# Performance work log

Hardware: AMD Instinct MI355X
Metric: run time of the kernel (lower is better)

The kernel has to match this reference:

```python
import jax, jax.numpy as jnp
import numpy as np

EPS = 1e-8  # torch CosineSimilarity default eps
IN_DIM = 4096
OUT_DIM = 32768
BATCH = 4096


def setup_inputs() -> dict:
    key = jax.random.key(0)
    kx, kw = jax.random.split(key)
    x = jax.random.normal(kx, (BATCH, IN_DIM), dtype=jnp.float32)
    # kaiming_normal_ on a (1, in, out) tensor: fan_in = in * out (last-dim fan), std = sqrt(2/fan_in)
    std = np.sqrt(2.0 / (IN_DIM * OUT_DIM)).astype(np.float32)
    weight = jax.random.normal(kw, (IN_DIM, OUT_DIM), dtype=jnp.float32) * std
    return {"x": x, "weight": weight}


def reference(x, weight):
    # cosine similarity along the in_dim axis between each row of x and each
    # column of weight: dot(x, w) / (max(||x||, eps) * max(||w||, eps))
    dots = jnp.einsum("bi,io->bo", x, weight)              # (B, out)
    x_norm = jnp.maximum(jnp.linalg.norm(x, axis=1), EPS)  # (B,)
    w_norm = jnp.maximum(jnp.linalg.norm(weight, axis=0), EPS)  # (out,)
    return dots / (x_norm[:, None] * w_norm[None, :])
```

## Files before the change

### kernel.cpp

```cpp
#include <hip/hip_runtime.h>
#include <hip/hip_bf16.h>
#include <cstdint>
#include <cstddef>

#define IN_DIM 4096
#define OUT_DIM 32768
#define BATCH 4096
#define EPS 1e-8f

typedef __attribute__((ext_vector_type(4))) float f32x4;
typedef __attribute__((ext_vector_type(8))) short bf16x8;

__device__ __forceinline__ unsigned short f2bf(float f) {
    union { float f; unsigned int u; } v;
    v.f = f;
    unsigned int u = v.u;
    unsigned int r = (u + 0x7FFFu + ((u >> 16) & 1u)) >> 16;
    return (unsigned short)r;
}

__device__ __forceinline__ void load_lds16(const void* g, void* l) {
    __builtin_amdgcn_global_load_lds(
        (const __attribute__((address_space(1))) void*)g,
        (__attribute__((address_space(3))) void*)l,
        16, 0, 0);
}

__global__ void xprep(const float* __restrict__ x,
                      unsigned short* __restrict__ xb,
                      float* __restrict__ xinv) {
    const int row = blockIdx.x;
    const int tid = threadIdx.x;
    const float4* x4 = (const float4*)(x + (size_t)row * IN_DIM);
    ushort4* xb4 = (ushort4*)(xb + (size_t)row * IN_DIM);
    float ss = 0.f;
#pragma unroll
    for (int it = 0; it < IN_DIM / 4 / 256; ++it) {
        int i = it * 256 + tid;
        float4 v = x4[i];
        ss += v.x * v.x + v.y * v.y + v.z * v.z + v.w * v.w;
        ushort4 o;
        o.x = f2bf(v.x); o.y = f2bf(v.y); o.z = f2bf(v.z); o.w = f2bf(v.w);
        xb4[i] = o;
    }
#pragma unroll
    for (int off = 32; off > 0; off >>= 1) ss += __shfl_down(ss, off);
    __shared__ float red[4];
    if ((tid & 63) == 0) red[tid >> 6] = ss;
    __syncthreads();
    if (tid == 0) {
        float s = red[0] + red[1] + red[2] + red[3];
        xinv[row] = 1.f / fmaxf(sqrtf(s), EPS);
    }
}

__global__ void wprep(const float* __restrict__ w,
                      unsigned short* __restrict__ wt,
                      float* __restrict__ wn2) {
    __shared__ unsigned short tile[64][66];
    __shared__ float colsum[64];
    const int t = threadIdx.x;
    const int j0 = blockIdx.x * 64;
    const int i0 = blockIdx.y * 64;
    if (t < 64) colsum[t] = 0.f;
    __syncthreads();

    const int jj = t & 63;
    const int ibase = t >> 6;
    float ss = 0.f;
#pragma unroll
    for (int it = 0; it < 16; ++it) {
        int ii = it * 4 + ibase;
        float v = w[(size_t)(i0 + ii) * OUT_DIM + j0 + jj];
        ss += v * v;
        tile[ii][jj] = f2bf(v);
    }
    atomicAdd(&colsum[jj], ss);
    __syncthreads();
    if (t < 64) atomicAdd(&wn2[j0 + t], colsum[t]);

    const int ii2 = t & 63;
    const int jbase = t >> 6;
#pragma unroll
    for (int it = 0; it < 16; ++it) {
        int jj2 = it * 4 + jbase;
        wt[(size_t)(j0 + jj2) * IN_DIM + i0 + ii2] = tile[ii2][jj2];
    }
}

__global__ void wfin(const float* __restrict__ wn2, float* __restrict__ winv) {
    int j = blockIdx.x * 256 + threadIdx.x;
    winv[j] = 1.f / fmaxf(sqrtf(wn2[j]), EPS);
}

#define BM 128
#define BN 128
#define BK 32

__global__ void gemm_kernel(const unsigned short* __restrict__ A,
                            const unsigned short* __restrict__ B,
                            float* __restrict__ C,
                            const float* __restrict__ xinv,
                            const float* __restrict__ winv) {
    __shared__ unsigned short As[BM * BK];
    __shared__ unsigned short Bs[BN * BK];

    const int tid = threadIdx.x;
    const int wave = tid >> 6;
    const int lane = tid & 63;
    const int m0 = blockIdx.x * BM;
    const int n0 = blockIdx.y * BN;
    const int wm = (wave & 1) * 64;
    const int wn = (wave >> 1) * 64;

    f32x4 acc[4][4] = {};

    const int lrow = lane >> 2;
    const int lk = (lane & 3) * 8;

    const int ml = lane & 15;
    const int quad = lane >> 4;

    for (int k0 = 0; k0 < IN_DIM; k0 += BK) {
#pragma unroll
        for (int l = 0; l < 2; ++l) {
            int grow = l * 64 + wave * 16 + lrow;
            const unsigned short* gpa = A + (size_t)(m0 + grow) * IN_DIM + k0 + lk;
            unsigned short* lpa = As + (size_t)(l * 256 + wave * 64) * 8;
            load_lds16(gpa, lpa);
            const unsigned short* gpb = B + (size_t)(n0 + grow) * IN_DIM + k0 + lk;
            unsigned short* lpb = Bs + (size_t)(l * 256 + wave * 64) * 8;
            load_lds16(gpb, lpb);
        }
        __syncthreads();

        bf16x8 af[4], bfr[4];
#pragma unroll
        for (int i = 0; i < 4; ++i) {
            af[i] = *(const bf16x8*)&As[(wm + i * 16 + ml) * BK + quad * 8];
            bfr[i] = *(const bf16x8*)&Bs[(wn + i * 16 + ml) * BK + quad * 8];
        }
#pragma unroll
        for (int i = 0; i < 4; ++i)
#pragma unroll
            for (int j = 0; j < 4; ++j)
                acc[i][j] = __builtin_amdgcn_mfma_f32_16x16x32_bf16(
                    af[i], bfr[j], acc[i][j], 0, 0, 0);
        __syncthreads();
    }

    float xs[4][4];
#pragma unroll
    for (int i = 0; i < 4; ++i)
#pragma unroll
        for (int r = 0; r < 4; ++r)
            xs[i][r] = xinv[m0 + wm + i * 16 + quad * 4 + r];

#pragma unroll
    for (int j = 0; j < 4; ++j) {
        int n = n0 + wn + j * 16 + ml;
        float wsc = winv[n];
#pragma unroll
        for (int i = 0; i < 4; ++i) {
            int mbase = m0 + wm + i * 16 + quad * 4;
#pragma unroll
            for (int r = 0; r < 4; ++r) {
                C[(size_t)(mbase + r) * OUT_DIM + n] = acc[i][j][r] * wsc * xs[i][r];
            }
        }
    }
}

extern "C" void kernel_launch(void* const* d_in, const int* in_sizes, int n_in,
                              void* d_out, int out_size, void* d_ws, size_t ws_size,
                              hipStream_t stream) {
    const float* x = (const float*)d_in[0];
    const float* w = (const float*)d_in[1];
    float* out = (float*)d_out;

    char* ws = (char*)d_ws;
    unsigned short* xb = (unsigned short*)ws;
    unsigned short* wt = (unsigned short*)(ws + (size_t)BATCH * IN_DIM * 2);
    char* tail = ws + (size_t)BATCH * IN_DIM * 2 + (size_t)OUT_DIM * IN_DIM * 2;
    float* xinv = (float*)tail;
    float* wn2 = xinv + BATCH;
    float* winv = wn2 + OUT_DIM;

    hipMemsetAsync(wn2, 0, OUT_DIM * sizeof(float), stream);
    xprep<<<BATCH, 256, 0, stream>>>(x, xb, xinv);
    wprep<<<dim3(OUT_DIM / 64, IN_DIM / 64), 256, 0, stream>>>(w, wt, wn2);
    wfin<<<OUT_DIM / 256, 256, 0, stream>>>(wn2, winv);
    gemm_kernel<<<dim3(BATCH / BM, OUT_DIM / BN), 256, 0, stream>>>(xb, wt, out, xinv, winv);
}
```

Baseline: 2.100 ms.

## Rewrite GEMM with 256x256 tiles, 4-stage LDS pipeline, swizzle; vectorize wprep

The GEMM moves to 256x256 block tiles with 8 waves, a 4-deep ring of LDS buffers filled by asynchronous global-to-LDS loads, and an XOR swizzle on LDS addresses to avoid bank conflicts. It also remaps block IDs for better L2 locality and raises wave priority around the MFMA sections. The weight prep kernel now uses float4 loads, packed 16-byte transposed stores and fewer atomics per column. The costs are 128KB of dynamic LDS per block, higher register pressure from the doubled accumulators, and complex hand-written wait counts that must be exactly right to stay correct.

```diff
diff --git a/kernel.cpp b/kernel.cpp
--- a/kernel.cpp
+++ b/kernel.cpp
@@ -10,6 +10,7 @@
 
 typedef __attribute__((ext_vector_type(4))) float f32x4;
 typedef __attribute__((ext_vector_type(8))) short bf16x8;
+typedef __attribute__((ext_vector_type(4))) unsigned int u32x4;
 
 __device__ __forceinline__ unsigned short f2bf(float f) {
     union { float f; unsigned int u; } v;
@@ -57,34 +58,59 @@
 __global__ void wprep(const float* __restrict__ w,
                       unsigned short* __restrict__ wt,
                       float* __restrict__ wn2) {
-    __shared__ unsigned short tile[64][66];
-    __shared__ float colsum[64];
+    __shared__ unsigned int tile32[64][33];
+    __shared__ f32x4 csum[256];
     const int t = threadIdx.x;
     const int j0 = blockIdx.x * 64;
-    const int i0 = blockIdx.y * 64;
-    if (t < 64) colsum[t] = 0.f;
+    const int kb = blockIdx.y * 512;
+    const int c4 = t & 15;
+    const int ir = t >> 4;
+    f32x4 ss = {0.f, 0.f, 0.f, 0.f};
+#pragma unroll 1
+    for (int tk = 0; tk < 8; ++tk) {
+        const int i0 = kb + tk * 64;
+#pragma unroll
+        for (int p = 0; p < 4; ++p) {
+            int il = p * 16 + ir;
+            const float4 v = *(const float4*)(w + (size_t)(i0 + il) * OUT_DIM + j0 + c4 * 4);
+            ss[0] += v.x * v.x; ss[1] += v.y * v.y;
+            ss[2] += v.z * v.z; ss[3] += v.w * v.w;
+            tile32[il][c4 * 2]     = (unsigned int)f2bf(v.x) | ((unsigned int)f2bf(v.y) << 16);
+            tile32[il][c4 * 2 + 1] = (unsigned int)f2bf(v.z) | ((unsigned int)f2bf(v.w) << 16);
+        }
+        __syncthreads();
+#pragma unroll
+        for (int e = 0; e < 2; ++e) {
+            int idx = e * 256 + t;
+            int jj = idx >> 3;
+            int ch = idx & 7;
+            unsigned int sh = (jj & 1) * 16;
+            int cc = jj >> 1;
+            unsigned int u0 = (tile32[ch * 8 + 0][cc] >> sh) & 0xffffu;
+            unsigned int u1 = (tile32[ch * 8 + 1][cc] >> sh) & 0xffffu;
+            unsigned int u2 = (tile32[ch * 8 + 2][cc] >> sh) & 0xffffu;
+            unsigned int u3 = (tile32[ch * 8 + 3][cc] >> sh) & 0xffffu;
+            unsigned int u4 = (tile32[ch * 8 + 4][cc] >> sh) & 0xffffu;
+            unsigned int u5 = (tile32[ch * 8 + 5][cc] >> sh) & 0xffffu;
+            unsigned int u6 = (tile32[ch * 8 + 6][cc] >> sh) & 0xffffu;
+            unsigned int u7 = (tile32[ch * 8 + 7][cc] >> sh) & 0xffffu;
+            u32x4 o;
+            o[0] = u0 | (u1 << 16); o[1] = u2 | (u3 << 16);
+            o[2] = u4 | (u5 << 16); o[3] = u6 | (u7 << 16);
+            *(u32x4*)(wt + (size_t)(j0 + jj) * IN_DIM + i0 + ch * 8) = o;
+        }
+        __syncthreads();
+    }
+    csum[t] = ss;
     __syncthreads();
-
-    const int jj = t & 63;
-    const int ibase = t >> 6;
-    float ss = 0.f;
-#pragma unroll
-    for (int it = 0; it < 16; ++it) {
-        int ii = it * 4 + ibase;
-        float v = w[(size_t)(i0 + ii) * OUT_DIM + j0 + jj];
-        ss += v * v;
-        tile[ii][jj] = f2bf(v);
-    }
-    atomicAdd(&colsum[jj], ss);
-    __syncthreads();
-    if (t < 64) atomicAdd(&wn2[j0 + t], colsum[t]);
-
-    const int ii2 = t & 63;
-    const int jbase = t >> 6;
-#pragma unroll
-    for (int it = 0; it < 16; ++it) {
-        int jj2 = it * 4 + jbase;
-        wt[(size_t)(j0 + jj2) * IN_DIM + i0 + ii2] = tile[ii2][jj2];
+    if (t < 16) {
+        f32x4 a = csum[t];
+#pragma unroll
+        for (int g = 1; g < 16; ++g) a += csum[t + 16 * g];
+        atomicAdd(&wn2[j0 + t * 4 + 0], a[0]);
+        atomicAdd(&wn2[j0 + t * 4 + 1], a[1]);
+        atomicAdd(&wn2[j0 + t * 4 + 2], a[2]);
+        atomicAdd(&wn2[j0 + t * 4 + 3], a[3]);
     }
 }
 
@@ -93,65 +119,137 @@
     winv[j] = 1.f / fmaxf(sqrtf(wn2[j]), EPS);
 }
 
-#define BM 128
-#define BN 128
+#define BM 256
+#define BN 256
 #define BK 32
-
+#define NT (IN_DIM / BK)
+#define TILE_BYTES 16384
+#define BUF_BYTES 32768
+
+__launch_bounds__(512, 2)
 __global__ void gemm_kernel(const unsigned short* __restrict__ A,
                             const unsigned short* __restrict__ B,
                             float* __restrict__ C,
                             const float* __restrict__ xinv,
                             const float* __restrict__ winv) {
-    __shared__ unsigned short As[BM * BK];
-    __shared__ unsigned short Bs[BN * BK];
-
+    extern __shared__ char smem[];
     const int tid = threadIdx.x;
     const int wave = tid >> 6;
     const int lane = tid & 63;
-    const int m0 = blockIdx.x * BM;
-    const int n0 = blockIdx.y * BN;
-    const int wm = (wave & 1) * 64;
-    const int wn = (wave >> 1) * 64;
-
-    f32x4 acc[4][4] = {};
-
-    const int lrow = lane >> 2;
-    const int lk = (lane & 3) * 8;
-
     const int ml = lane & 15;
     const int quad = lane >> 4;
 
-    for (int k0 = 0; k0 < IN_DIM; k0 += BK) {
-#pragma unroll
-        for (int l = 0; l < 2; ++l) {
-            int grow = l * 64 + wave * 16 + lrow;
-            const unsigned short* gpa = A + (size_t)(m0 + grow) * IN_DIM + k0 + lk;
-            unsigned short* lpa = As + (size_t)(l * 256 + wave * 64) * 8;
-            load_lds16(gpa, lpa);
-            const unsigned short* gpb = B + (size_t)(n0 + grow) * IN_DIM + k0 + lk;
-            unsigned short* lpb = Bs + (size_t)(l * 256 + wave * 64) * 8;
-            load_lds16(gpb, lpb);
-        }
-        __syncthreads();
+    const int bid = blockIdx.x;
+    const int swz = (bid & 7) * 256 + (bid >> 3);
+    const int m0 = (swz & 15) * BM;
+    const int n0 = (swz >> 4) * BN;
+
+    const int wm = (wave >> 2) * 128;
+    const int wn = (wave & 3) * 64;
+
+    const int p0 = tid;
+    const int Ra = p0 >> 2, Qa = p0 & 3;
+    const int r0b = (Ra ^ (Ra >> 2)) & 1;
+    const int rA0 = (Ra & ~1) | r0b;
+    const int qA0 = Qa ^ ((Ra & 2) | r0b);
+    const int p1 = tid + 512;
+    const int Rb = p1 >> 2, Qb = p1 & 3;
+    const int r1b = (Rb ^ (Rb >> 2)) & 1;
+    const int rA1 = (Rb & ~1) | r1b;
+    const int qA1 = Qb ^ ((Rb & 2) | r1b);
+
+    const unsigned short* gA0 = A + (size_t)(m0 + rA0) * IN_DIM + qA0 * 8;
+    const unsigned short* gA1 = A + (size_t)(m0 + rA1) * IN_DIM + qA1 * 8;
+    const unsigned short* gB0 = B + (size_t)(n0 + rA0) * IN_DIM + qA0 * 8;
+    const unsigned short* gB1 = B + (size_t)(n0 + rA1) * IN_DIM + qA1 * 8;
+
+    const int dst0 = wave * 1024;
+    const int dst1 = 8192 + wave * 1024;
+
+    const int sw = (((ml & 7) ^ quad) << 4);
+    const int aoff = ((wm + ml) << 6) ^ sw;
+    const int boff = ((wn + ml) << 6) ^ sw;
+
+    f32x4 acc[8][4] = {};
+
+#pragma unroll
+    for (int tt = 0; tt < 3; ++tt) {
+        char* sb = smem + tt * BUF_BYTES;
+        load_lds16(gA0 + tt * BK, sb + dst0);
+        load_lds16(gA1 + tt * BK, sb + dst1);
+        load_lds16(gB0 + tt * BK, sb + TILE_BYTES + dst0);
+        load_lds16(gB1 + tt * BK, sb + TILE_BYTES + dst1);
+    }
+    asm volatile("s_waitcnt vmcnt(8)" ::: "memory");
+    __builtin_amdgcn_sched_barrier(0);
+    __builtin_amdgcn_s_barrier();
+    __builtin_amdgcn_sched_barrier(0);
+
+    int koff = 3 * BK;
+    for (int t = 0; t < NT; ++t) {
+        const char* ta = smem + (t & 3) * BUF_BYTES;
+        const char* tb = ta + TILE_BYTES;
+        char* sb = smem + ((t + 3) & 3) * BUF_BYTES;
+        const bool st = (t + 3) < NT;
 
         bf16x8 af[4], bfr[4];
 #pragma unroll
-        for (int i = 0; i < 4; ++i) {
-            af[i] = *(const bf16x8*)&As[(wm + i * 16 + ml) * BK + quad * 8];
-            bfr[i] = *(const bf16x8*)&Bs[(wn + i * 16 + ml) * BK + quad * 8];
-        }
+        for (int i = 0; i < 4; ++i)
+            af[i] = *(const bf16x8*)(ta + aoff + i * 1024);
+#pragma unroll
+        for (int j = 0; j < 4; ++j)
+            bfr[j] = *(const bf16x8*)(tb + boff + j * 1024);
+        if (st) {
+            load_lds16(gA0 + koff, sb + dst0);
+            load_lds16(gA1 + koff, sb + dst1);
+        }
+        __builtin_amdgcn_s_barrier();
+        asm volatile("s_waitcnt lgkmcnt(0)" ::: "memory");
+        __builtin_amdgcn_s_setprio(1);
 #pragma unroll
         for (int i = 0; i < 4; ++i)
 #pragma unroll
             for (int j = 0; j < 4; ++j)
                 acc[i][j] = __builtin_amdgcn_mfma_f32_16x16x32_bf16(
                     af[i], bfr[j], acc[i][j], 0, 0, 0);
-        __syncthreads();
-    }
-
-    float xs[4][4];
-#pragma unroll
-    for (int i = 0; i < 4; ++i)
+        __builtin_amdgcn_s_setprio(0);
+        __builtin_amdgcn_s_barrier();
+
+        bf16x8 ag[4];
+#pragma unroll
+        for (int i = 0; i < 4; ++i)
+            ag[i] = *(const bf16x8*)(ta + aoff + 4096 + i * 1024);
+        if (st) {
+            load_lds16(gB0 + koff, sb + TILE_BYTES + dst0);
+            load_lds16(gB1 + koff, sb + TILE_BYTES + dst1);
+        }
+        __builtin_amdgcn_s_barrier();
+        asm volatile("s_waitcnt lgkmcnt(0)" ::: "memory");
+        __builtin_amdgcn_s_setprio(1);
+#pragma unroll
+        for (int i = 0; i < 4; ++i)
+#pragma unroll
+            for (int j = 0; j < 4; ++j)
+                acc[4 + i][j] = __builtin_amdgcn_mfma_f32_16x16x32_bf16(
+                    ag[i], bfr[j], acc[4 + i][j], 0, 0, 0);
+        __builtin_amdgcn_s_setprio(0);
+
+        if (t < NT - 3) {
+            asm volatile("s_waitcnt vmcnt(8)" ::: "memory");
+        } else if (t == NT - 3) {
+            asm volatile("s_waitcnt vmcnt(4)" ::: "memory");
+        } else if (t == NT - 2) {
+            asm volatile("s_waitcnt vmcnt(0)" ::: "memory");
+        }
+        __builtin_amdgcn_sched_barrier(0);
+        __builtin_amdgcn_s_barrier();
+        __builtin_amdgcn_sched_barrier(0);
+        koff += BK;
+    }
+
+    float xs[8][4];
+#pragma unroll
+    for (int i = 0; i < 8; ++i)
 #pragma unroll
         for (int r = 0; r < 4; ++r)
             xs[i][r] = xinv[m0 + wm + i * 16 + quad * 4 + r];
@@ -161,7 +259,7 @@
         int n = n0 + wn + j * 16 + ml;
         float wsc = winv[n];
 #pragma unroll
-        for (int i = 0; i < 4; ++i) {
+        for (int i = 0; i < 8; ++i) {
             int mbase = m0 + wm + i * 16 + quad * 4;
 #pragma unroll
             for (int r = 0; r < 4; ++r) {
@@ -188,7 +286,11 @@
 
     hipMemsetAsync(wn2, 0, OUT_DIM * sizeof(float), stream);
     xprep<<<BATCH, 256, 0, stream>>>(x, xb, xinv);
-    wprep<<<dim3(OUT_DIM / 64, IN_DIM / 64), 256, 0, stream>>>(w, wt, wn2);
+    wprep<<<dim3(OUT_DIM / 64, IN_DIM / 512), 256, 0, stream>>>(w, wt, wn2);
     wfin<<<OUT_DIM / 256, 256, 0, stream>>>(wn2, winv);
-    gemm_kernel<<<dim3(BATCH / BM, OUT_DIM / BN), 256, 0, stream>>>(xb, wt, out, xinv, winv);
-}
+
+    hipFuncSetAttribute((const void*)gemm_kernel,
+                        hipFuncAttributeMaxDynamicSharedMemorySize, 131072);
+    gemm_kernel<<<(BATCH / BM) * (OUT_DIM / BN), 512, 131072, stream>>>(
+        xb, wt, out, xinv, winv);
+}
```

New measurement: 1.992 ms. 5.2% less time.
